# Kernel optimization log

Measured on AMD Instinct MI355X. Metric: run time of the kernel, lower is better.

Reference implementation:

```python
import jax, jax.numpy as jnp
import numpy as np

N = 100000
F_IN = 256
F_OUT = 128
E = 1600000


def setup_inputs() -> dict:
    key = jax.random.key(0)
    k1, k2, k3, k4 = jax.random.split(key, 4)
    x = jax.random.normal(k1, (N, F_IN), dtype=jnp.float32)
    edge_index = jax.random.randint(k2, (2, E), 0, N, dtype=jnp.int64)
    # GCNConv parameters (glorot-ish init) + PReLU per-channel slope (torch default 0.25)
    W = jax.random.normal(k3, (F_IN, F_OUT), dtype=jnp.float32) / np.sqrt(F_IN)
    bias = jnp.zeros((F_OUT,), dtype=jnp.float32)
    prelu_a = jnp.full((F_OUT,), 0.25, dtype=jnp.float32)
    return {"x": x, "edge_index": edge_index, "W": W, "bias": bias, "prelu_a": prelu_a}


def reference(x, edge_index, W, bias, prelu_a):
    n = x.shape[0]
    # PyG GCNConv: linear transform first
    h = x @ W  # [N, F_OUT]
    # add self-loops (GCNConv default add_self_loops=True)
    loop = jnp.arange(n, dtype=edge_index.dtype)
    row = jnp.concatenate([edge_index[0], loop])  # source
    col = jnp.concatenate([edge_index[1], loop])  # target
    # symmetric degree normalization: deg over targets with unit edge weights
    ones = jnp.ones(row.shape[0], dtype=h.dtype)
    deg = jax.ops.segment_sum(ones, col, num_segments=n)
    deg_inv_sqrt = jnp.where(deg > 0, jax.lax.rsqrt(deg), 0.0)
    norm = deg_inv_sqrt[row] * deg_inv_sqrt[col]  # [E+N]
    # gather-normalize-scatter aggregation
    msgs = h[row] * norm[:, None]  # [E+N, F_OUT]
    out = jax.ops.segment_sum(msgs, col, num_segments=n) + bias  # [N, F_OUT]
    # PReLU with per-channel slope
    z = jnp.where(out > 0, out, prelu_a * out)
    return z
```

## Files before the change

kernel.cpp:

```cpp
#include <hip/hip_runtime.h>

#define N_NODES 100000
#define F_IN    256
#define F_OUT   128
#define N_EDGES 1600000

#define BSH       8
#define NBUCK     ((N_NODES + 255) >> 8)
#define K1_BLOCKS 256
#define K3_BLOCKS 250
#define K3_Q      (N_EDGES / 4 / K3_BLOCKS)

typedef unsigned int   uint;
typedef unsigned char  uchar;
typedef unsigned short ushort;
typedef short  s16x8 __attribute__((ext_vector_type(8)));
typedef float  f32x4 __attribute__((ext_vector_type(4)));

__device__ __forceinline__ ushort f2bf(float f) {
    uint b = __float_as_uint(f);
    b += 0x7FFFu + ((b >> 16) & 1u);
    return (ushort)(b >> 16);
}
__device__ __forceinline__ float bf2f(uint h16) {
    return __uint_as_float(h16 << 16);
}

__global__ __launch_bounds__(256) void bcount_kernel(const int* __restrict__ ei,
                                                     int* __restrict__ bcnt) {
    __shared__ int h[NBUCK];
    for (int i = threadIdx.x; i < NBUCK; i += 256) h[i] = 0;
    __syncthreads();
    const int4* tgt = (const int4*)&ei[N_EDGES];
    const int total = N_EDGES / 4;
    for (int i = blockIdx.x * 256 + threadIdx.x; i < total; i += K1_BLOCKS * 256) {
        const int4 v = tgt[i];
        atomicAdd(&h[v.x >> BSH], 1);
        atomicAdd(&h[v.y >> BSH], 1);
        atomicAdd(&h[v.z >> BSH], 1);
        atomicAdd(&h[v.w >> BSH], 1);
    }
    __syncthreads();
    for (int i = threadIdx.x; i < NBUCK; i += 256) {
        const int c = h[i];
        if (c) atomicAdd(&bcnt[i], c);
    }
}

__global__ __launch_bounds__(512) void bscan_kernel(const int* __restrict__ bcnt,
                                                    int* __restrict__ bstart,
                                                    int* __restrict__ gcur) {
    __shared__ int s[512];
    const int t = threadIdx.x;
    const int c = (t < NBUCK) ? bcnt[t] : 0;
    s[t] = c;
    __syncthreads();
    for (int o = 1; o < 512; o <<= 1) {
        const int add = (t >= o) ? s[t - o] : 0;
        __syncthreads();
        s[t] += add;
        __syncthreads();
    }
    if (t < NBUCK) {
        const int excl = s[t] - c;
        bstart[t] = excl;
        gcur[t]   = excl;
        if (t == NBUCK - 1) bstart[NBUCK] = s[t];
    }
}

__global__ __launch_bounds__(256) void bscatter_kernel(const int* __restrict__ ei,
                                                       int* __restrict__ gcur,
                                                       int* __restrict__ ebuf) {
    __shared__ __align__(16) int tv[K3_Q * 4];
    __shared__ int h[NBUCK];
    for (int i = threadIdx.x; i < NBUCK; i += 256) h[i] = 0;
    __syncthreads();
    const int g0 = blockIdx.x * K3_Q;
    const int4* tgt = (const int4*)&ei[N_EDGES];
    const int4* src = (const int4*)&ei[0];
    for (int q = threadIdx.x; q < K3_Q; q += 256) {
        const int4 v = tgt[g0 + q];
        atomicAdd(&h[v.x >> BSH], 1);
        atomicAdd(&h[v.y >> BSH], 1);
        atomicAdd(&h[v.z >> BSH], 1);
        atomicAdd(&h[v.w >> BSH], 1);
        *(int4*)&tv[q * 4] = v;
    }
    __syncthreads();
    for (int i = threadIdx.x; i < NBUCK; i += 256) {
        const int c = h[i];
        h[i] = c ? atomicAdd(&gcur[i], c) : 0;
    }
    __syncthreads();
    for (int q = threadIdx.x; q < K3_Q; q += 256) {
        const int4 u = src[g0 + q];
        const int4 v = *(const int4*)&tv[q * 4];
        const int s0 = atomicAdd(&h[v.x >> BSH], 1);
        const int s1 = atomicAdd(&h[v.y >> BSH], 1);
        const int s2 = atomicAdd(&h[v.z >> BSH], 1);
        const int s3 = atomicAdd(&h[v.w >> BSH], 1);
        ebuf[s0] = ((v.x & 255) << 17) | u.x;
        ebuf[s1] = ((v.y & 255) << 17) | u.y;
        ebuf[s2] = ((v.z & 255) << 17) | u.z;
        ebuf[s3] = ((v.w & 255) << 17) | u.w;
    }
}

__global__ __launch_bounds__(256) void build_kernel(const int* __restrict__ bstart,
                                                    const int* __restrict__ ebuf,
                                                    int* __restrict__ adj,
                                                    int* __restrict__ count,
                                                    int* __restrict__ off,
                                                    float* __restrict__ dinv) {
    __shared__ int cnt[256];
    __shared__ int scan[256];
    const int b  = blockIdx.x;
    const int t  = threadIdx.x;
    const int e0 = bstart[b];
    const int e1 = bstart[b + 1];
    cnt[t] = 0;
    __syncthreads();
    for (int i = e0 + t; i < e1; i += 256)
        atomicAdd(&cnt[(ebuf[i] >> 17) & 255], 1);
    __syncthreads();
    const int val = cnt[t];
    scan[t] = val;
    __syncthreads();
    for (int o = 1; o < 256; o <<= 1) {
        const int add = (t >= o) ? scan[t - o] : 0;
        __syncthreads();
        scan[t] += add;
        __syncthreads();
    }
    const int excl = scan[t] - val;
    const int v = (b << BSH) + t;
    if (v < N_NODES) {
        off[v]   = e0 + excl;
        count[v] = val;
        dinv[v]  = rsqrtf((float)(val + 1));
    }
    cnt[t] = excl;
    __syncthreads();
    for (int i = e0 + t; i < e1; i += 256) {
        const int key  = ebuf[i];
        const int slot = atomicAdd(&cnt[(key >> 17) & 255], 1);
        adj[e0 + slot] = key & 0x1FFFF;
    }
}

__global__ __launch_bounds__(256) void wpack_kernel(const float* __restrict__ W,
                                                    ushort* __restrict__ Wp) {
    const int gid = blockIdx.x * 256 + threadIdx.x;
    const int lane = gid & 63;
    const int s    = (gid >> 6) & 7;
    const int t    = gid >> 9;
    const int krow = s * 32 + (lane >> 4) * 8;
    const int col  = t * 16 + (lane & 15);
    ushort h[8];
#pragma unroll
    for (int j = 0; j < 8; ++j)
        h[j] = f2bf(W[(krow + j) * F_OUT + col]);
    ushort* dst = &Wp[(size_t)gid * 8];
#pragma unroll
    for (int j = 0; j < 8; ++j) dst[j] = h[j];
}

__global__ __launch_bounds__(256) void mfma_gemm_kernel(const float* __restrict__ x,
                                                        const s16x8* __restrict__ Wp,
                                                        const float* __restrict__ dinv,
                                                        ushort* __restrict__ g16) {
    const int tid  = threadIdx.x;
    const int wave = tid >> 6;
    const int lane = tid & 63;
    const int aq   = lane >> 4;
    const int al   = lane & 15;

    const int row_base = blockIdx.x * 64 + wave * 16;
    const int arow = row_base + al;
    const int arow_c = arow < N_NODES ? arow : N_NODES - 1;
    const float* xrow = &x[(size_t)arow_c * F_IN + aq * 8];

    f32x4 acc[8] = {};

#pragma unroll
    for (int s = 0; s < 8; ++s) {
        const float4 a0 = *(const float4*)&xrow[s * 32];
        const float4 a1 = *(const float4*)&xrow[s * 32 + 4];
        s16x8 af;
        af[0] = (short)f2bf(a0.x); af[1] = (short)f2bf(a0.y);
        af[2] = (short)f2bf(a0.z); af[3] = (short)f2bf(a0.w);
        af[4] = (short)f2bf(a1.x); af[5] = (short)f2bf(a1.y);
        af[6] = (short)f2bf(a1.z); af[7] = (short)f2bf(a1.w);
#pragma unroll
        for (int t = 0; t < 8; ++t) {
            const s16x8 bf = Wp[(t * 8 + s) * 64 + lane];
            acc[t] = __builtin_amdgcn_mfma_f32_16x16x32_bf16(af, bf, acc[t], 0, 0, 0);
        }
    }

    const int rrow0 = row_base + aq * 4;
    const float4 dv = *(const float4*)&dinv[rrow0];
    const float dvr[4] = {dv.x, dv.y, dv.z, dv.w};
#pragma unroll
    for (int r = 0; r < 4; ++r) {
        const int row = rrow0 + r;
        if (row < N_NODES) {
            ushort* orow = &g16[(size_t)row * F_OUT];
#pragma unroll
            for (int t = 0; t < 8; ++t)
                orow[t * 16 + al] = f2bf(acc[t][r] * dvr[r]);
        }
    }
}

__global__ __launch_bounds__(256) void aggregate_kernel(const int* __restrict__ count,
                                                        const int* __restrict__ off,
                                                        const float* __restrict__ dinv,
                                                        const int* __restrict__ adj,
                                                        const ushort* __restrict__ g16,
                                                        const float* __restrict__ bias,
                                                        const float* __restrict__ prelu_a,
                                                        float* __restrict__ out) {
    const int tid  = threadIdx.x;
    const int lane = tid & 31;
    const int v    = blockIdx.x * 8 + (tid >> 5);
    if (v >= N_NODES) return;
    const int f = lane * 4;

    const uint2 sv = *(const uint2*)&g16[(size_t)v * F_OUT + f];
    float a0 = bf2f(sv.x & 0xFFFFu);
    float a1 = bf2f(sv.x >> 16);
    float a2 = bf2f(sv.y & 0xFFFFu);
    float a3 = bf2f(sv.y >> 16);

    const int c = count[v];
    const int* adj_v = &adj[off[v]];

    int i = 0;
    for (; i + 4 <= c; i += 4) {
        const int u0 = adj_v[i];
        const int u1 = adj_v[i + 1];
        const int u2 = adj_v[i + 2];
        const int u3 = adj_v[i + 3];
        const uint2 r0 = *(const uint2*)&g16[(size_t)u0 * F_OUT + f];
        const uint2 r1 = *(const uint2*)&g16[(size_t)u1 * F_OUT + f];
        const uint2 r2 = *(const uint2*)&g16[(size_t)u2 * F_OUT + f];
        const uint2 r3 = *(const uint2*)&g16[(size_t)u3 * F_OUT + f];
        a0 += bf2f(r0.x & 0xFFFFu) + bf2f(r1.x & 0xFFFFu) + bf2f(r2.x & 0xFFFFu) + bf2f(r3.x & 0xFFFFu);
        a1 += bf2f(r0.x >> 16)     + bf2f(r1.x >> 16)     + bf2f(r2.x >> 16)     + bf2f(r3.x >> 16);
        a2 += bf2f(r0.y & 0xFFFFu) + bf2f(r1.y & 0xFFFFu) + bf2f(r2.y & 0xFFFFu) + bf2f(r3.y & 0xFFFFu);
        a3 += bf2f(r0.y >> 16)     + bf2f(r1.y >> 16)     + bf2f(r2.y >> 16)     + bf2f(r3.y >> 16);
    }
    for (; i < c; ++i) {
        const int u0 = adj_v[i];
        const uint2 r0 = *(const uint2*)&g16[(size_t)u0 * F_OUT + f];
        a0 += bf2f(r0.x & 0xFFFFu);
        a1 += bf2f(r0.x >> 16);
        a2 += bf2f(r0.y & 0xFFFFu);
        a3 += bf2f(r0.y >> 16);
    }

    const float s = dinv[v];
    const float4 bi = *(const float4*)&bias[f];
    const float4 pa = *(const float4*)&prelu_a[f];
    float4 o;
    o.x = a0 * s + bi.x;
    o.y = a1 * s + bi.y;
    o.z = a2 * s + bi.z;
    o.w = a3 * s + bi.w;
    o.x = o.x > 0.f ? o.x : pa.x * o.x;
    o.y = o.y > 0.f ? o.y : pa.y * o.y;
    o.z = o.z > 0.f ? o.z : pa.z * o.z;
    o.w = o.w > 0.f ? o.w : pa.w * o.w;
    *(float4*)&out[(size_t)v * F_OUT + f] = o;
}

extern "C" void kernel_launch(void* const* d_in, const int* in_sizes, int n_in,
                              void* d_out, int out_size, void* d_ws, size_t ws_size,
                              hipStream_t stream) {
    const float* x    = (const float*)d_in[0];
    const int*   ei   = (const int*)d_in[1];
    const float* W    = (const float*)d_in[2];
    const float* bias = (const float*)d_in[3];
    const float* pa   = (const float*)d_in[4];
    float* out = (float*)d_out;

    char* ws = (char*)d_ws;
    int*    count  = (int*)ws;
    float*  dinv   = (float*)(ws + 400384);
    int*    off    = (int*)(ws + 800768);
    int*    bcnt   = (int*)(ws + 1201152);
    int*    bstart = (int*)(ws + 1203200);
    int*    gcur   = (int*)(ws + 1205248);
    int*    adj    = (int*)(ws + 1207296);
    ushort* g16    = (ushort*)(ws + 7607296);
    int*    ebuf   = (int*)(ws + 7607296);
    ushort* Wp     = (ushort*)(ws + 33207296);

    hipMemsetAsync(bcnt, 0, 2048, stream);

    wpack_kernel<<<16, 256, 0, stream>>>(W, Wp);
    bcount_kernel<<<K1_BLOCKS, 256, 0, stream>>>(ei, bcnt);
    bscan_kernel<<<1, 512, 0, stream>>>(bcnt, bstart, gcur);
    bscatter_kernel<<<K3_BLOCKS, 256, 0, stream>>>(ei, gcur, ebuf);
    build_kernel<<<NBUCK, 256, 0, stream>>>(bstart, ebuf, adj, count, off, dinv);
    mfma_gemm_kernel<<<(N_NODES + 63) / 64, 256, 0, stream>>>(x, (const s16x8*)Wp, dinv, g16);
    aggregate_kernel<<<(N_NODES + 7) / 8, 256, 0, stream>>>(count, off, dinv, adj, g16, bias, pa, out);
}
```

Measured before the change: 307.4 us.

## Pad bucket counters, widen CSR build and aggregation, add more blocks

Spaces the global bucket counters 16 ints apart so atomics on neighbouring buckets stop sharing cache lines, and raises the block counts of the count and scatter kernels fourfold. The per-bucket build kernel now runs with 1024 threads. Aggregation switches to 16 lanes per node with 16-byte bf16 loads, an 8-way unrolled neighbour loop and cheaper bf16-to-float unpacking. These changes target atomic contention, low parallelism in preprocessing and memory-level parallelism in the gather, but raise per-thread register use and move the workspace offsets.

```diff
diff --git a/kernel.cpp b/kernel.cpp
--- a/kernel.cpp
+++ b/kernel.cpp
@@ -7,8 +7,9 @@
 
 #define BSH       8
 #define NBUCK     ((N_NODES + 255) >> 8)
-#define K1_BLOCKS 256
-#define K3_BLOCKS 250
+#define CPAD      16
+#define K1_BLOCKS 1024
+#define K3_BLOCKS 1000
 #define K3_Q      (N_EDGES / 4 / K3_BLOCKS)
 
 typedef unsigned int   uint;
@@ -43,7 +44,7 @@
     __syncthreads();
     for (int i = threadIdx.x; i < NBUCK; i += 256) {
         const int c = h[i];
-        if (c) atomicAdd(&bcnt[i], c);
+        if (c) atomicAdd(&bcnt[i * CPAD], c);
     }
 }
 
@@ -52,7 +53,7 @@
                                                     int* __restrict__ gcur) {
     __shared__ int s[512];
     const int t = threadIdx.x;
-    const int c = (t < NBUCK) ? bcnt[t] : 0;
+    const int c = (t < NBUCK) ? bcnt[t * CPAD] : 0;
     s[t] = c;
     __syncthreads();
     for (int o = 1; o < 512; o <<= 1) {
@@ -63,8 +64,8 @@
     }
     if (t < NBUCK) {
         const int excl = s[t] - c;
-        bstart[t] = excl;
-        gcur[t]   = excl;
+        bstart[t]       = excl;
+        gcur[t * CPAD]  = excl;
         if (t == NBUCK - 1) bstart[NBUCK] = s[t];
     }
 }
@@ -90,7 +91,7 @@
     __syncthreads();
     for (int i = threadIdx.x; i < NBUCK; i += 256) {
         const int c = h[i];
-        h[i] = c ? atomicAdd(&gcur[i], c) : 0;
+        h[i] = c ? atomicAdd(&gcur[i * CPAD], c) : 0;
     }
     __syncthreads();
     for (int q = threadIdx.x; q < K3_Q; q += 256) {
@@ -107,42 +108,45 @@
     }
 }
 
-__global__ __launch_bounds__(256) void build_kernel(const int* __restrict__ bstart,
-                                                    const int* __restrict__ ebuf,
-                                                    int* __restrict__ adj,
-                                                    int* __restrict__ count,
-                                                    int* __restrict__ off,
-                                                    float* __restrict__ dinv) {
+__global__ __launch_bounds__(1024) void build_kernel(const int* __restrict__ bstart,
+                                                     const int* __restrict__ ebuf,
+                                                     int* __restrict__ adj,
+                                                     int* __restrict__ count,
+                                                     int* __restrict__ off,
+                                                     float* __restrict__ dinv) {
     __shared__ int cnt[256];
     __shared__ int scan[256];
     const int b  = blockIdx.x;
     const int t  = threadIdx.x;
     const int e0 = bstart[b];
     const int e1 = bstart[b + 1];
-    cnt[t] = 0;
-    __syncthreads();
-    for (int i = e0 + t; i < e1; i += 256)
+    if (t < 256) cnt[t] = 0;
+    __syncthreads();
+    for (int i = e0 + t; i < e1; i += 1024)
         atomicAdd(&cnt[(ebuf[i] >> 17) & 255], 1);
     __syncthreads();
-    const int val = cnt[t];
-    scan[t] = val;
+    const int val = (t < 256) ? cnt[t] : 0;
+    if (t < 256) scan[t] = val;
     __syncthreads();
     for (int o = 1; o < 256; o <<= 1) {
-        const int add = (t >= o) ? scan[t - o] : 0;
+        int add = 0;
+        if (t < 256 && t >= o) add = scan[t - o];
         __syncthreads();
-        scan[t] += add;
+        if (t < 256) scan[t] += add;
         __syncthreads();
     }
-    const int excl = scan[t] - val;
-    const int v = (b << BSH) + t;
-    if (v < N_NODES) {
-        off[v]   = e0 + excl;
-        count[v] = val;
-        dinv[v]  = rsqrtf((float)(val + 1));
-    }
-    cnt[t] = excl;
-    __syncthreads();
-    for (int i = e0 + t; i < e1; i += 256) {
+    if (t < 256) {
+        const int excl = scan[t] - val;
+        const int v = (b << BSH) + t;
+        if (v < N_NODES) {
+            off[v]   = e0 + excl;
+            count[v] = val;
+            dinv[v]  = rsqrtf((float)(val + 1));
+        }
+        cnt[t] = excl;
+    }
+    __syncthreads();
+    for (int i = e0 + t; i < e1; i += 1024) {
         const int key  = ebuf[i];
         const int slot = atomicAdd(&cnt[(key >> 17) & 255], 1);
         adj[e0 + slot] = key & 0x1FFFF;
@@ -214,6 +218,12 @@
     }
 }
 
+#define ACC8(r) \
+    a0 += __uint_as_float((r).x << 16); a1 += __uint_as_float((r).x & 0xFFFF0000u); \
+    a2 += __uint_as_float((r).y << 16); a3 += __uint_as_float((r).y & 0xFFFF0000u); \
+    a4 += __uint_as_float((r).z << 16); a5 += __uint_as_float((r).z & 0xFFFF0000u); \
+    a6 += __uint_as_float((r).w << 16); a7 += __uint_as_float((r).w & 0xFFFF0000u);
+
 __global__ __launch_bounds__(256) void aggregate_kernel(const int* __restrict__ count,
                                                         const int* __restrict__ off,
                                                         const float* __restrict__ dinv,
@@ -222,58 +232,76 @@
                                                         const float* __restrict__ bias,
                                                         const float* __restrict__ prelu_a,
                                                         float* __restrict__ out) {
-    const int tid  = threadIdx.x;
-    const int lane = tid & 31;
-    const int v    = blockIdx.x * 8 + (tid >> 5);
+    const int tid = threadIdx.x;
+    const int l   = tid & 15;
+    const int v   = blockIdx.x * 16 + (tid >> 4);
     if (v >= N_NODES) return;
-    const int f = lane * 4;
-
-    const uint2 sv = *(const uint2*)&g16[(size_t)v * F_OUT + f];
-    float a0 = bf2f(sv.x & 0xFFFFu);
-    float a1 = bf2f(sv.x >> 16);
-    float a2 = bf2f(sv.y & 0xFFFFu);
-    float a3 = bf2f(sv.y >> 16);
+    const int f   = l * 8;
+
+    const uint4 sv = *(const uint4*)&g16[(uint)v * F_OUT + f];
+    float a0 = bf2f(sv.x & 0xFFFFu), a1 = __uint_as_float(sv.x & 0xFFFF0000u);
+    float a2 = bf2f(sv.y & 0xFFFFu), a3 = __uint_as_float(sv.y & 0xFFFF0000u);
+    float a4 = bf2f(sv.z & 0xFFFFu), a5 = __uint_as_float(sv.z & 0xFFFF0000u);
+    float a6 = bf2f(sv.w & 0xFFFFu), a7 = __uint_as_float(sv.w & 0xFFFF0000u);
 
     const int c = count[v];
     const int* adj_v = &adj[off[v]];
 
     int i = 0;
+    for (; i + 8 <= c; i += 8) {
+        const int u0 = adj_v[i + 0], u1 = adj_v[i + 1], u2 = adj_v[i + 2], u3 = adj_v[i + 3];
+        const int u4 = adj_v[i + 4], u5 = adj_v[i + 5], u6 = adj_v[i + 6], u7 = adj_v[i + 7];
+        const uint4 r0 = *(const uint4*)&g16[(uint)u0 * F_OUT + f];
+        const uint4 r1 = *(const uint4*)&g16[(uint)u1 * F_OUT + f];
+        const uint4 r2 = *(const uint4*)&g16[(uint)u2 * F_OUT + f];
+        const uint4 r3 = *(const uint4*)&g16[(uint)u3 * F_OUT + f];
+        const uint4 r4 = *(const uint4*)&g16[(uint)u4 * F_OUT + f];
+        const uint4 r5 = *(const uint4*)&g16[(uint)u5 * F_OUT + f];
+        const uint4 r6 = *(const uint4*)&g16[(uint)u6 * F_OUT + f];
+        const uint4 r7 = *(const uint4*)&g16[(uint)u7 * F_OUT + f];
+        ACC8(r0); ACC8(r1); ACC8(r2); ACC8(r3);
+        ACC8(r4); ACC8(r5); ACC8(r6); ACC8(r7);
+    }
     for (; i + 4 <= c; i += 4) {
+        const int u0 = adj_v[i + 0], u1 = adj_v[i + 1], u2 = adj_v[i + 2], u3 = adj_v[i + 3];
+        const uint4 r0 = *(const uint4*)&g16[(uint)u0 * F_OUT + f];
+        const uint4 r1 = *(const uint4*)&g16[(uint)u1 * F_OUT + f];
+        const uint4 r2 = *(const uint4*)&g16[(uint)u2 * F_OUT + f];
+        const uint4 r3 = *(const uint4*)&g16[(uint)u3 * F_OUT + f];
+        ACC8(r0); ACC8(r1); ACC8(r2); ACC8(r3);
+    }
+    for (; i + 2 <= c; i += 2) {
+        const int u0 = adj_v[i + 0], u1 = adj_v[i + 1];
+        const uint4 r0 = *(const uint4*)&g16[(uint)u0 * F_OUT + f];
+        const uint4 r1 = *(const uint4*)&g16[(uint)u1 * F_OUT + f];
+        ACC8(r0); ACC8(r1);
+    }
+    if (i < c) {
         const int u0 = adj_v[i];
-        const int u1 = adj_v[i + 1];
-        const int u2 = adj_v[i + 2];
-        const int u3 = adj_v[i + 3];
-        const uint2 r0 = *(const uint2*)&g16[(size_t)u0 * F_OUT + f];
-        const uint2 r1 = *(const uint2*)&g16[(size_t)u1 * F_OUT + f];
-        const uint2 r2 = *(const uint2*)&g16[(size_t)u2 * F_OUT + f];
-        const uint2 r3 = *(const uint2*)&g16[(size_t)u3 * F_OUT + f];
-        a0 += bf2f(r0.x & 0xFFFFu) + bf2f(r1.x & 0xFFFFu) + bf2f(r2.x & 0xFFFFu) + bf2f(r3.x & 0xFFFFu);
-        a1 += bf2f(r0.x >> 16)     + bf2f(r1.x >> 16)     + bf2f(r2.x >> 16)     + bf2f(r3.x >> 16);
-        a2 += bf2f(r0.y & 0xFFFFu) + bf2f(r1.y & 0xFFFFu) + bf2f(r2.y & 0xFFFFu) + bf2f(r3.y & 0xFFFFu);
-        a3 += bf2f(r0.y >> 16)     + bf2f(r1.y >> 16)     + bf2f(r2.y >> 16)     + bf2f(r3.y >> 16);
-    }
-    for (; i < c; ++i) {
-        const int u0 = adj_v[i];
-        const uint2 r0 = *(const uint2*)&g16[(size_t)u0 * F_OUT + f];
-        a0 += bf2f(r0.x & 0xFFFFu);
-        a1 += bf2f(r0.x >> 16);
-        a2 += bf2f(r0.y & 0xFFFFu);
-        a3 += bf2f(r0.y >> 16);
+        const uint4 r0 = *(const uint4*)&g16[(uint)u0 * F_OUT + f];
+        ACC8(r0);
     }
 
     const float s = dinv[v];
-    const float4 bi = *(const float4*)&bias[f];
-    const float4 pa = *(const float4*)&prelu_a[f];
-    float4 o;
-    o.x = a0 * s + bi.x;
-    o.y = a1 * s + bi.y;
-    o.z = a2 * s + bi.z;
-    o.w = a3 * s + bi.w;
-    o.x = o.x > 0.f ? o.x : pa.x * o.x;
-    o.y = o.y > 0.f ? o.y : pa.y * o.y;
-    o.z = o.z > 0.f ? o.z : pa.z * o.z;
-    o.w = o.w > 0.f ? o.w : pa.w * o.w;
-    *(float4*)&out[(size_t)v * F_OUT + f] = o;
+    const float4 bi0 = *(const float4*)&bias[f];
+    const float4 bi1 = *(const float4*)&bias[f + 4];
+    const float4 pa0 = *(const float4*)&prelu_a[f];
+    const float4 pa1 = *(const float4*)&prelu_a[f + 4];
+    float4 o0, o1;
+    o0.x = a0 * s + bi0.x;  o0.y = a1 * s + bi0.y;
+    o0.z = a2 * s + bi0.z;  o0.w = a3 * s + bi0.w;
+    o1.x = a4 * s + bi1.x;  o1.y = a5 * s + bi1.y;
+    o1.z = a6 * s + bi1.z;  o1.w = a7 * s + bi1.w;
+    o0.x = o0.x > 0.f ? o0.x : pa0.x * o0.x;
+    o0.y = o0.y > 0.f ? o0.y : pa0.y * o0.y;
+    o0.z = o0.z > 0.f ? o0.z : pa0.z * o0.z;
+    o0.w = o0.w > 0.f ? o0.w : pa0.w * o0.w;
+    o1.x = o1.x > 0.f ? o1.x : pa1.x * o1.x;
+    o1.y = o1.y > 0.f ? o1.y : pa1.y * o1.y;
+    o1.z = o1.z > 0.f ? o1.z : pa1.z * o1.z;
+    o1.w = o1.w > 0.f ? o1.w : pa1.w * o1.w;
+    *(float4*)&out[(uint)v * F_OUT + f]     = o0;
+    *(float4*)&out[(uint)v * F_OUT + f + 4] = o1;
 }
 
 extern "C" void kernel_launch(void* const* d_in, const int* in_sizes, int n_in,
@@ -291,20 +319,20 @@
     float*  dinv   = (float*)(ws + 400384);
     int*    off    = (int*)(ws + 800768);
     int*    bcnt   = (int*)(ws + 1201152);
-    int*    bstart = (int*)(ws + 1203200);
-    int*    gcur   = (int*)(ws + 1205248);
-    int*    adj    = (int*)(ws + 1207296);
-    ushort* g16    = (ushort*)(ws + 7607296);
-    int*    ebuf   = (int*)(ws + 7607296);
-    ushort* Wp     = (ushort*)(ws + 33207296);
-
-    hipMemsetAsync(bcnt, 0, 2048, stream);
+    int*    bstart = (int*)(ws + 1226240);
+    int*    gcur   = (int*)(ws + 1228288);
+    int*    adj    = (int*)(ws + 1253376);
+    ushort* g16    = (ushort*)(ws + 7653376);
+    int*    ebuf   = (int*)(ws + 7653376);
+    ushort* Wp     = (ushort*)(ws + 33253376);
+
+    hipMemsetAsync(bcnt, 0, 25088, stream);
 
     wpack_kernel<<<16, 256, 0, stream>>>(W, Wp);
     bcount_kernel<<<K1_BLOCKS, 256, 0, stream>>>(ei, bcnt);
     bscan_kernel<<<1, 512, 0, stream>>>(bcnt, bstart, gcur);
     bscatter_kernel<<<K3_BLOCKS, 256, 0, stream>>>(ei, gcur, ebuf);
-    build_kernel<<<NBUCK, 256, 0, stream>>>(bstart, ebuf, adj, count, off, dinv);
+    build_kernel<<<NBUCK, 1024, 0, stream>>>(bstart, ebuf, adj, count, off, dinv);
     mfma_gemm_kernel<<<(N_NODES + 63) / 64, 256, 0, stream>>>(x, (const s16x8*)Wp, dinv, g16);
-    aggregate_kernel<<<(N_NODES + 7) / 8, 256, 0, stream>>>(count, off, dinv, adj, g16, bias, pa, out);
-}
+    aggregate_kernel<<<(N_NODES + 15) / 16, 256, 0, stream>>>(count, off, dinv, adj, g16, bias, pa, out);
+}
```

Result: slower. 341.0 us (+10.9%).
